# Performance work log

Measured on AMD Instinct MI355X. Metric: run time of the kernel, lower is better.

The kernel has to match this reference:

```python
import jax, jax.numpy as jnp
import numpy as np

N_HEADS = 2
WINDOW = 4
BLOCK = 256


def _get_rel_emb(emb, length):
    # emb: [1, 2*WINDOW+1, K] -> [1, 2*length-1, K]
    pad = max(length - (WINDOW + 1), 0)
    start = max((WINDOW + 1) - length, 0)
    e = jnp.pad(emb, ((0, 0), (pad, pad), (0, 0)))
    return e[:, start:start + 2 * length - 1]


def _rel_to_abs(x):
    # x: [b, h, l, 2l-1] -> [b, h, l, l] (skew trick)
    b, h, l, _ = x.shape
    x = jnp.pad(x, ((0, 0), (0, 0), (0, 0), (0, 1))).reshape(b, h, 2 * l * l)
    x = jnp.pad(x, ((0, 0), (0, 0), (0, l - 1))).reshape(b, h, l + 1, 2 * l - 1)
    return x[:, :, :l, l - 1:]


def _abs_to_rel(x):
    # x: [b, h, l, l] -> [b, h, l, 2l-1] (inverse skew)
    b, h, l, _ = x.shape
    x = jnp.pad(x, ((0, 0), (0, 0), (0, 0), (0, l - 1))).reshape(b, h, l * (2 * l - 1))
    x = jnp.pad(x, ((0, 0), (0, 0), (l, 0))).reshape(b, h, l, 2 * l)
    return x[:, :, :, 1:]


def _attention(x, c, attn_mask, Wq, bq, Wk, bk, Wv, bv, Wo, bo, emb_rel_k, emb_rel_v):
    B, C, T = x.shape
    H, K = N_HEADS, C // N_HEADS
    # projections (torch Linear on [B,T,C])
    q = (jnp.einsum('bct,cd->btd', x, Wq) + bq).reshape(B, T, H, K).transpose(0, 2, 1, 3)
    k = (jnp.einsum('bct,cd->btd', c, Wk) + bk).reshape(B, T, H, K).transpose(0, 2, 1, 3)
    v = (jnp.einsum('bct,cd->btd', c, Wv) + bv).reshape(B, T, H, K).transpose(0, 2, 1, 3)
    qs = q / jnp.sqrt(jnp.float32(K))
    scores = jnp.einsum('bhtk,bhsk->bhts', qs, k)  # [B,H,T,T]
    # relative-position key logits (heads_share=True -> single table)
    rel_k = _get_rel_emb(emb_rel_k, T)[0]          # [2T-1, K]
    rel_logits = jnp.einsum('bhtk,rk->bhtr', qs, rel_k)
    scores = scores + _rel_to_abs(rel_logits)
    # proximal bias: -log1p(|i-j|)
    r = jnp.arange(T, dtype=jnp.float32)
    scores = scores - jnp.log1p(jnp.abs(r[:, None] - r[None, :]))[None, None]
    # attn mask + block-local mask (block mask active because mask is given)
    ij = jnp.arange(T)
    block_ok = jnp.abs(ij[:, None] - ij[None, :]) <= BLOCK
    valid = (attn_mask != 0) & block_ok[None, None]
    scores = jnp.where(valid, scores, jnp.float32(-1e4))
    p = jax.nn.softmax(scores, axis=-1)
    out = jnp.einsum('bhts,bhsk->bhtk', p, v)
    # relative-position value contribution
    rel_v = _get_rel_emb(emb_rel_v, T)[0]          # [2T-1, K]
    out = out + jnp.einsum('bhtr,rk->bhtk', _abs_to_rel(p), rel_v)
    out = out.transpose(0, 2, 1, 3).reshape(B, T, C)
    y = jnp.einsum('btd,do->bto', out, Wo) + bo
    return y.transpose(0, 2, 1)  # [B, out_channels, T]


def setup_inputs() -> dict:
    key = jax.random.key(0)
    ks = jax.random.split(key, 8)
    B, C, T = 4, 192, 2048
    K = C // N_HEADS
    s = jnp.float32(0.05)
    rel_std = jnp.float32(K ** -0.5)
    return {
        'x': jax.random.normal(ks[0], (B, C, T), jnp.float32),
        'c': jax.random.normal(ks[1], (B, C, T), jnp.float32),
        'Wq': jax.random.normal(ks[2], (C, C), jnp.float32) * s,
        'bq': jnp.zeros((C,), jnp.float32),
        'Wk': jax.random.normal(ks[3], (C, C), jnp.float32) * s,
        'bk': jnp.zeros((C,), jnp.float32),
        'Wv': jax.random.normal(ks[4], (C, C), jnp.float32) * s,
        'bv': jnp.zeros((C,), jnp.float32),
        'Wo': jax.random.normal(ks[5], (C, C), jnp.float32) * s,
        'bo': jnp.zeros((C,), jnp.float32),
        'emb_rel_k': jax.random.normal(ks[6], (1, 2 * WINDOW + 1, K), jnp.float32) * rel_std,
        'emb_rel_v': jax.random.normal(ks[7], (1, 2 * WINDOW + 1, K), jnp.float32) * rel_std,
        'attn_mask': jnp.ones((B, 1, T, T), jnp.int32),
    }


def reference(x, c, Wq, bq, Wk, bk, Wv, bv, Wo, bo, emb_rel_k, emb_rel_v, attn_mask):
    return _attention(x, c, attn_mask, Wq, bq, Wk, bk, Wv, bv, Wo, bo, emb_rel_k, emb_rel_v)
```

## Files before the change

### kernel.cpp

```cpp
#include <hip/hip_runtime.h>
#include <hip/hip_bf16.h>

#define B_DIM 4
#define C_DIM 192
#define T_SEQ 2048
#define H_DIM 2
#define K_DIM 96
#define BAND 256
#define IT 16
#define WSLOT 544
#define W_P 548
#define PMW 17

typedef __attribute__((ext_vector_type(8))) short bf16x8;
typedef __attribute__((ext_vector_type(4))) short bf16x4;
typedef __attribute__((ext_vector_type(4))) float f32x4;
#define MFMA16 __builtin_amdgcn_mfma_f32_16x16x32_bf16

__device__ __forceinline__ float bf2f(__hip_bfloat16 v) { return __bfloat162float(v); }
__device__ __forceinline__ float bfbits2f(short s) {
    union { short s; __hip_bfloat16 h; } u; u.s = s; return __bfloat162float(u.h);
}
__device__ __forceinline__ short f2bf_bits(float f) {
    union { __hip_bfloat16 h; short s; } u; u.h = __float2bfloat16(f); return u.s;
}

#define OFF_WT(m)  ((size_t)(m)*73728)
#define OFF_BQS    ((size_t)294912)
#define OFF_PM     ((size_t)295680)
#define OFF_QBF    ((size_t)852736)
#define OFF_KBF    (OFF_QBF + 3145728)
#define OFF_VTB    (OFF_KBF + 3145728)
#define OFF_OBTC   (OFF_VTB + 3145728)

__global__ __launch_bounds__(256)
void prep_w_kernel(const float* __restrict__ Wq, const float* __restrict__ Wk,
                   const float* __restrict__ Wv, const float* __restrict__ Wo,
                   const float* __restrict__ bq, char* __restrict__ ws)
{
    const float qscale = 0.10206207261596577f;
    const size_t idx = (size_t)blockIdx.x*256 + threadIdx.x;
    if (blockIdx.x == 576) {
        if (threadIdx.x < C_DIM)
            ((float*)(ws + OFF_BQS))[threadIdx.x] = bq[threadIdx.x]*qscale;
        return;
    }
    const int mi  = (int)(idx / 36864);
    const int rem = (int)(idx % 36864);
    const int d = rem / C_DIM, c = rem % C_DIM;
    const float* src = (mi == 0) ? Wq : (mi == 1) ? Wk : (mi == 2) ? Wv : Wo;
    float v = src[c*C_DIM + d];
    if (mi == 0) v *= qscale;
    ((short*)(ws + OFF_WT(mi)))[d*C_DIM + c] = f2bf_bits(v);
}

__global__ __launch_bounds__(256)
void pack_mask_kernel(const int* __restrict__ mask, char* __restrict__ ws)
{
    const int idx = blockIdx.x*256 + threadIdx.x;
    const int b = idx / (T_SEQ*PMW);
    const int rem = idx % (T_SEQ*PMW);
    const int i = rem / PMW, w = rem % PMW;
    const int jlo = max(0, (i & ~15) - BAND);
    const int* mrow = mask + ((size_t)b*T_SEQ + i)*T_SEQ;
    unsigned bits = 0;
    #pragma unroll
    for (int g4 = 0; g4 < 8; ++g4) {
        const int jg = jlo + 32*w + 4*g4;
        if (jg + 3 < T_SEQ) {
            const int4 mv = *reinterpret_cast<const int4*>(mrow + jg);
            bits |= (unsigned)(mv.x != 0) << (4*g4);
            bits |= (unsigned)(mv.y != 0) << (4*g4+1);
            bits |= (unsigned)(mv.z != 0) << (4*g4+2);
            bits |= (unsigned)(mv.w != 0) << (4*g4+3);
        } else {
            #pragma unroll
            for (int e = 0; e < 4; ++e)
                if (jg + e < T_SEQ && mrow[jg+e] != 0) bits |= 1u << (4*g4+e);
        }
    }
    ((unsigned*)(ws + OFF_PM))[idx] = bits;
}

__global__ __launch_bounds__(256)
void proj_kernel(const float* __restrict__ x, const float* __restrict__ cin,
                 const float* __restrict__ bk, const float* __restrict__ bv,
                 char* __restrict__ ws)
{
    __shared__ short xs[IT*C_DIM];
    __shared__ short cs[IT*C_DIM];
    const int b   = blockIdx.x >> 7;
    const int t0  = (blockIdx.x & 127) * IT;
    const int tid = threadIdx.x;
    const int wave = tid >> 6, lane = tid & 63;
    const int q4 = lane >> 4, lr = lane & 15;

    if (tid < C_DIM) {
        const int c = tid;
        const float* xp = x   + ((size_t)(b*C_DIM + c))*T_SEQ + t0;
        const float* cp = cin + ((size_t)(b*C_DIM + c))*T_SEQ + t0;
        union { float4 f4[4]; float f[16]; } xu, cu;
        #pragma unroll
        for (int u = 0; u < 4; ++u) {
            xu.f4[u] = *reinterpret_cast<const float4*>(xp + 4*u);
            cu.f4[u] = *reinterpret_cast<const float4*>(cp + 4*u);
        }
        #pragma unroll
        for (int tt = 0; tt < IT; ++tt) {
            xs[tt*C_DIM + c] = f2bf_bits(xu.f[tt]);
            cs[tt*C_DIM + c] = f2bf_bits(cu.f[tt]);
        }
    }
    __syncthreads();

    const short* WqT = (const short*)(ws + OFF_WT(0));
    const short* WkT = (const short*)(ws + OFF_WT(1));
    const short* WvT = (const short*)(ws + OFF_WT(2));

    f32x4 qa[3], ka[3], va[3];
    #pragma unroll
    for (int j = 0; j < 3; ++j) {
        qa[j] = (f32x4){0,0,0,0}; ka[j] = (f32x4){0,0,0,0}; va[j] = (f32x4){0,0,0,0};
    }
    for (int kc = 0; kc < 6; ++kc) {
        const int ko = kc*32 + q4*8;
        const bf16x8 xf = *reinterpret_cast<const bf16x8*>(xs + lr*C_DIM + ko);
        const bf16x8 cf = *reinterpret_cast<const bf16x8*>(cs + lr*C_DIM + ko);
        #pragma unroll
        for (int j = 0; j < 3; ++j) {
            const int dt = 3*wave + j;
            const bf16x8 wqf = *reinterpret_cast<const bf16x8*>(WqT + (dt*16 + lr)*C_DIM + ko);
            const bf16x8 wkf = *reinterpret_cast<const bf16x8*>(WkT + (dt*16 + lr)*C_DIM + ko);
            const bf16x8 wvf = *reinterpret_cast<const bf16x8*>(WvT + (dt*16 + lr)*C_DIM + ko);
            qa[j] = MFMA16(xf, wqf, qa[j], 0, 0, 0);
            ka[j] = MFMA16(cf, wkf, ka[j], 0, 0, 0);
            va[j] = MFMA16(wvf, cf, va[j], 0, 0, 0);
        }
    }

    const float* bqs = (const float*)(ws + OFF_BQS);
    short* qbf = (short*)(ws + OFF_QBF);
    short* kbf = (short*)(ws + OFF_KBF);
    short* vtb = (short*)(ws + OFF_VTB);
    #pragma unroll
    for (int j = 0; j < 3; ++j) {
        const int dt = 3*wave + j;
        {
            const int d = dt*16 + lr, h = d/K_DIM, kk = d%K_DIM;
            const int bh = b*H_DIM + h;
            const float bq_v = bqs[d], bk_v = bk[d];
            #pragma unroll
            for (int e = 0; e < 4; ++e) {
                const int t = t0 + q4*4 + e;
                const size_t off = ((size_t)bh*T_SEQ + t)*K_DIM + kk;
                qbf[off] = f2bf_bits(qa[j][e] + bq_v);
                kbf[off] = f2bf_bits(ka[j][e] + bk_v);
            }
        }
        {
            #pragma unroll
            for (int e = 0; e < 4; ++e) {
                const int d = dt*16 + q4*4 + e, h = d/K_DIM, kk = d%K_DIM;
                const int bh = b*H_DIM + h;
                vtb[((size_t)bh*K_DIM + kk)*T_SEQ + t0 + lr] = f2bf_bits(va[j][e] + bv[d]);
            }
        }
    }
}

__global__ __launch_bounds__(256)
void attn_kernel(const float* __restrict__ relk, const float* __restrict__ relv,
                 char* __restrict__ ws)
{
    __shared__ float p_s[IT*W_P];
    __shared__ float shbuf[864];

    const short* qbf = (const short*)(ws + OFF_QBF);
    const short* kbf = (const short*)(ws + OFF_KBF);
    const short* vtb = (const short*)(ws + OFF_VTB);
    const unsigned* pm = (const unsigned*)(ws + OFF_PM);
    short* obtc = (short*)(ws + OFF_OBTC);

    const int bh  = blockIdx.x >> 7;
    const int i0  = (blockIdx.x & 127) * IT;
    const int b   = bh / H_DIM;
    const int h   = bh % H_DIM;
    const int tid = threadIdx.x;
    const int wave = tid >> 6, lane = tid & 63;
    const int q4 = lane >> 4, lr = lane & 15;

    const int jlo  = max(0, i0 - BAND);
    const int jhi  = min(T_SEQ - 1, i0 + IT - 1 + BAND);
    const int wlen = jhi - jlo + 1;
    const size_t qkv_base = (size_t)bh * T_SEQ * K_DIM;

    float* lt = shbuf;
    float* rl = shbuf + 260;
    for (int idx = tid; idx < 257; idx += 256) lt[idx] = log1pf((float)idx);
    if (tid < IT*9) {
        const int r = tid/9, dd = tid%9;
        const short* qrow = qbf + qkv_base + (size_t)(i0 + r)*K_DIM;
        float s = 0.f;
        for (int k = 0; k < K_DIM; ++k)
            s += bfbits2f(qrow[k]) * relk[dd*K_DIM + k];
        rl[tid] = s;
    }

    bf16x8 qa[3];
    {
        const short* qrow = qbf + qkv_base + (size_t)(i0 + lr)*K_DIM + q4*8;
        #pragma unroll
        for (int kc = 0; kc < 3; ++kc)
            qa[kc] = *reinterpret_cast<const bf16x8*>(qrow + kc*32);
    }

    for (int jt = wave; jt < WSLOT/16; jt += 4) {
        int jr = jlo + jt*16 + lr;
        if (jr > T_SEQ-1) jr = T_SEQ-1;
        const short* krow = kbf + qkv_base + (size_t)jr*K_DIM + q4*8;
        f32x4 s = {0.f,0.f,0.f,0.f};
        #pragma unroll
        for (int kc = 0; kc < 3; ++kc)
            s = MFMA16(qa[kc], *reinterpret_cast<const bf16x8*>(krow + kc*32), s, 0, 0, 0);
        #pragma unroll
        for (int e = 0; e < 4; ++e)
            p_s[(q4*4 + e)*W_P + jt*16 + lr] = s[e];
    }
    __syncthreads();

    {
        const int r = tid >> 4, sj = tid & 15;
        const int i = i0 + r;
        const int pmrow = (b*T_SEQ + i)*PMW;
        float vals[36];
        float m = -INFINITY;
        #pragma unroll
        for (int mm = 0; mm < 9; ++mm) {
            const int j0 = 4*sj + 64*mm;
            float4 pv = make_float4(0.f,0.f,0.f,0.f);
            unsigned mb = 0;
            if (j0 < WSLOT) {
                pv = *reinterpret_cast<const float4*>(p_s + r*W_P + j0);
                mb = pm[pmrow + (j0 >> 5)] >> (j0 & 31);
            }
            const float pe[4] = {pv.x, pv.y, pv.z, pv.w};
            #pragma unroll
            for (int e = 0; e < 4; ++e) {
                const int j = j0 + e;
                float val = -INFINITY;
                if (j0 < WSLOT && j < wlen) {
                    const int jg = jlo + j, dd = jg - i;
                    const int ad = dd < 0 ? -dd : dd;
                    if (ad <= BAND && ((mb >> e) & 1)) {
                        val = pe[e] - lt[ad];
                        if ((unsigned)(dd + 4) <= 8u) val += rl[r*9 + dd + 4];
                    }
                }
                vals[mm*4 + e] = val;
                m = fmaxf(m, val);
            }
        }
        #pragma unroll
        for (int off = 8; off > 0; off >>= 1) m = fmaxf(m, __shfl_xor(m, off, 64));
        if (m == -INFINITY) m = 0.f;
        float ssum = 0.f;
        #pragma unroll
        for (int u = 0; u < 36; ++u) { vals[u] = __expf(vals[u] - m); ssum += vals[u]; }
        #pragma unroll
        for (int off = 8; off > 0; off >>= 1) ssum += __shfl_xor(ssum, off, 64);
        const float inv = ssum > 0.f ? 1.f/ssum : 0.f;
        short* pb = (short*)p_s;
        #pragma unroll
        for (int mm = 0; mm < 9; ++mm) {
            const int j0 = 4*sj + 64*mm;
            if (j0 < WSLOT) {
                bf16x4 w;
                #pragma unroll
                for (int e = 0; e < 4; ++e) w[e] = f2bf_bits(vals[mm*4+e]*inv);
                *reinterpret_cast<bf16x4*>(pb + r*(2*W_P) + j0) = w;
            }
        }
    }
    __syncthreads();

    for (int idx = tid; idx < 9*K_DIM; idx += 256) shbuf[idx] = relv[idx];

    const short* pb = (const short*)p_s;
    f32x4 o0 = {0.f,0.f,0.f,0.f}, o1 = {0.f,0.f,0.f,0.f};
    for (int kc = 0; kc < WSLOT/32; ++kc) {
        const bf16x8 pa = *reinterpret_cast<const bf16x8*>(pb + lr*(2*W_P) + kc*32 + q4*8);
        int tc = jlo + kc*32 + q4*8;
        if (tc > T_SEQ-8) tc = T_SEQ-8;
        const bf16x8 vb0 = *reinterpret_cast<const bf16x8*>(
            vtb + qkv_base + (size_t)(wave*16 + lr)*T_SEQ + tc);
        o0 = MFMA16(pa, vb0, o0, 0, 0, 0);
        if (wave < 2) {
            const bf16x8 vb1 = *reinterpret_cast<const bf16x8*>(
                vtb + qkv_base + (size_t)((wave+4)*16 + lr)*T_SEQ + tc);
            o1 = MFMA16(pa, vb1, o1, 0, 0, 0);
        }
    }
    __syncthreads();

    #pragma unroll
    for (int u = 0; u < 2; ++u) {
        if (u == 1 && wave >= 2) break;
        const int nt = (u == 0) ? wave : wave + 4;
        const f32x4 oc = (u == 0) ? o0 : o1;
        const int col = nt*16 + lr;
        #pragma unroll
        for (int e = 0; e < 4; ++e) {
            const int row = q4*4 + e;
            const int i = i0 + row;
            float v = oc[e];
            #pragma unroll
            for (int dd = 0; dd < 9; ++dd) {
                const int jg = i + dd - 4;
                if (jg >= 0 && jg < T_SEQ)
                    v += bfbits2f(pb[row*(2*W_P) + (jg - jlo)]) * shbuf[dd*K_DIM + col];
            }
            obtc[((size_t)b*T_SEQ + i)*C_DIM + h*K_DIM + col] = f2bf_bits(v);
        }
    }
}

__global__ __launch_bounds__(256)
void oproj_kernel(const float* __restrict__ bo, float* __restrict__ y,
                  const char* __restrict__ ws)
{
    const int b   = blockIdx.x >> 7;
    const int t0  = (blockIdx.x & 127) * 16;
    const int tid = threadIdx.x;
    const int wave = tid >> 6, lane = tid & 63;
    const int q4 = lane >> 4, lr = lane & 15;

    const short* WoT  = (const short*)(ws + OFF_WT(3));
    const short* obtc = (const short*)(ws + OFF_OBTC);

    f32x4 a[3];
    #pragma unroll
    for (int j = 0; j < 3; ++j) a[j] = (f32x4){0.f,0.f,0.f,0.f};
    for (int kc = 0; kc < 6; ++kc) {
        const int ko = kc*32 + q4*8;
        const bf16x8 bf = *reinterpret_cast<const bf16x8*>(
            obtc + ((size_t)b*T_SEQ + t0 + lr)*C_DIM + ko);
        #pragma unroll
        for (int j = 0; j < 3; ++j) {
            const bf16x8 af = *reinterpret_cast<const bf16x8*>(
                WoT + ((3*wave + j)*16 + lr)*C_DIM + ko);
            a[j] = MFMA16(af, bf, a[j], 0, 0, 0);
        }
    }
    #pragma unroll
    for (int j = 0; j < 3; ++j) {
        #pragma unroll
        for (int e = 0; e < 4; ++e) {
            const int d = (3*wave + j)*16 + q4*4 + e;
            y[((size_t)b*C_DIM + d)*T_SEQ + t0 + lr] = a[j][e] + bo[d];
        }
    }
}

extern "C" void kernel_launch(void* const* d_in, const int* in_sizes, int n_in,
                              void* d_out, int out_size, void* d_ws, size_t ws_size,
                              hipStream_t stream)
{
    const float* x    = (const float*)d_in[0];
    const float* c    = (const float*)d_in[1];
    const float* Wq   = (const float*)d_in[2];
    const float* bq   = (const float*)d_in[3];
    const float* Wk   = (const float*)d_in[4];
    const float* bk   = (const float*)d_in[5];
    const float* Wv   = (const float*)d_in[6];
    const float* bv   = (const float*)d_in[7];
    const float* Wo   = (const float*)d_in[8];
    const float* bo   = (const float*)d_in[9];
    const float* relk = (const float*)d_in[10];
    const float* relv = (const float*)d_in[11];
    const int*   mask = (const int*)d_in[12];
    float*       y    = (float*)d_out;
    char*        ws   = (char*)d_ws;

    hipLaunchKernelGGL(prep_w_kernel, dim3(577), dim3(256), 0, stream,
                       Wq, Wk, Wv, Wo, bq, ws);
    hipLaunchKernelGGL(pack_mask_kernel, dim3(544), dim3(256), 0, stream, mask, ws);
    hipLaunchKernelGGL(proj_kernel, dim3(B_DIM*(T_SEQ/16)), dim3(256), 0, stream,
                       x, c, bk, bv, ws);
    hipLaunchKernelGGL(attn_kernel, dim3(B_DIM*H_DIM*(T_SEQ/IT)), dim3(256), 0, stream,
                       relk, relv, ws);
    hipLaunchKernelGGL(oproj_kernel, dim3(B_DIM*(T_SEQ/16)), dim3(256), 0, stream,
                       bo, y, ws);
}
```

Measured before the change: 191.3 us.

## Merge prep kernels, compute relative-key logits with MFMA, spread input loads

Fuses the weight-prep and mask-packing kernels into one launch that also converts the relative-key table to padded bf16. In the attention kernel, the scalar 96-step dot products for the 9 relative-key logits become a single MFMA tile issued by one wave. The projection kernel now spreads its input loads over all 256 threads instead of 192. The weight-transpose index mapping changes so reads are coalesced and writes strided. The intent is to cut launch overhead and serial scalar work, at the cost of one wave doing extra MFMA work and padding the table to 16 rows.

```diff
diff --git a/kernel.cpp b/kernel.cpp
--- a/kernel.cpp
+++ b/kernel.cpp
@@ -17,7 +17,6 @@
 typedef __attribute__((ext_vector_type(4))) float f32x4;
 #define MFMA16 __builtin_amdgcn_mfma_f32_16x16x32_bf16
 
-__device__ __forceinline__ float bf2f(__hip_bfloat16 v) { return __bfloat162float(v); }
 __device__ __forceinline__ float bfbits2f(short s) {
     union { short s; __hip_bfloat16 h; } u; u.s = s; return __bfloat162float(u.h);
 }
@@ -27,59 +26,67 @@
 
 #define OFF_WT(m)  ((size_t)(m)*73728)
 #define OFF_BQS    ((size_t)294912)
-#define OFF_PM     ((size_t)295680)
-#define OFF_QBF    ((size_t)852736)
+#define OFF_RELKBF ((size_t)295680)
+#define OFF_PM     ((size_t)298752)
+#define OFF_QBF    ((size_t)855808)
 #define OFF_KBF    (OFF_QBF + 3145728)
 #define OFF_VTB    (OFF_KBF + 3145728)
 #define OFF_OBTC   (OFF_VTB + 3145728)
 
 __global__ __launch_bounds__(256)
-void prep_w_kernel(const float* __restrict__ Wq, const float* __restrict__ Wk,
-                   const float* __restrict__ Wv, const float* __restrict__ Wo,
-                   const float* __restrict__ bq, char* __restrict__ ws)
+void prep_kernel(const float* __restrict__ Wq, const float* __restrict__ Wk,
+                 const float* __restrict__ Wv, const float* __restrict__ Wo,
+                 const float* __restrict__ bq, const float* __restrict__ relk,
+                 const int* __restrict__ mask, char* __restrict__ ws)
 {
     const float qscale = 0.10206207261596577f;
-    const size_t idx = (size_t)blockIdx.x*256 + threadIdx.x;
-    if (blockIdx.x == 576) {
-        if (threadIdx.x < C_DIM)
-            ((float*)(ws + OFF_BQS))[threadIdx.x] = bq[threadIdx.x]*qscale;
+    const int bidx = blockIdx.x;
+    const int tid  = threadIdx.x;
+
+    if (bidx < 576) {
+        const size_t idx = (size_t)bidx*256 + tid;
+        const int mi  = (int)(idx / 36864);
+        const int rem = (int)(idx % 36864);
+        const int c = rem / C_DIM, d = rem % C_DIM;
+        const float* src = (mi == 0) ? Wq : (mi == 1) ? Wk : (mi == 2) ? Wv : Wo;
+        float v = src[c*C_DIM + d];
+        if (mi == 0) v *= qscale;
+        ((short*)(ws + OFF_WT(mi)))[d*C_DIM + c] = f2bf_bits(v);
         return;
     }
-    const int mi  = (int)(idx / 36864);
-    const int rem = (int)(idx % 36864);
-    const int d = rem / C_DIM, c = rem % C_DIM;
-    const float* src = (mi == 0) ? Wq : (mi == 1) ? Wk : (mi == 2) ? Wv : Wo;
-    float v = src[c*C_DIM + d];
-    if (mi == 0) v *= qscale;
-    ((short*)(ws + OFF_WT(mi)))[d*C_DIM + c] = f2bf_bits(v);
-}
-
-__global__ __launch_bounds__(256)
-void pack_mask_kernel(const int* __restrict__ mask, char* __restrict__ ws)
-{
-    const int idx = blockIdx.x*256 + threadIdx.x;
-    const int b = idx / (T_SEQ*PMW);
-    const int rem = idx % (T_SEQ*PMW);
-    const int i = rem / PMW, w = rem % PMW;
-    const int jlo = max(0, (i & ~15) - BAND);
-    const int* mrow = mask + ((size_t)b*T_SEQ + i)*T_SEQ;
-    unsigned bits = 0;
-    #pragma unroll
-    for (int g4 = 0; g4 < 8; ++g4) {
-        const int jg = jlo + 32*w + 4*g4;
-        if (jg + 3 < T_SEQ) {
-            const int4 mv = *reinterpret_cast<const int4*>(mrow + jg);
-            bits |= (unsigned)(mv.x != 0) << (4*g4);
-            bits |= (unsigned)(mv.y != 0) << (4*g4+1);
-            bits |= (unsigned)(mv.z != 0) << (4*g4+2);
-            bits |= (unsigned)(mv.w != 0) << (4*g4+3);
-        } else {
-            #pragma unroll
-            for (int e = 0; e < 4; ++e)
-                if (jg + e < T_SEQ && mrow[jg+e] != 0) bits |= 1u << (4*g4+e);
-        }
-    }
-    ((unsigned*)(ws + OFF_PM))[idx] = bits;
+    if (bidx < 1120) {
+        const int idx = (bidx - 576)*256 + tid;
+        const int b = idx / (T_SEQ*PMW);
+        const int rem = idx % (T_SEQ*PMW);
+        const int i = rem / PMW, w = rem % PMW;
+        const int jlo = max(0, (i & ~15) - BAND);
+        const int* mrow = mask + ((size_t)b*T_SEQ + i)*T_SEQ;
+        unsigned bits = 0;
+        #pragma unroll
+        for (int g4 = 0; g4 < 8; ++g4) {
+            const int jg = jlo + 32*w + 4*g4;
+            if (jg + 3 < T_SEQ) {
+                const int4 mv = *reinterpret_cast<const int4*>(mrow + jg);
+                bits |= (unsigned)(mv.x != 0) << (4*g4);
+                bits |= (unsigned)(mv.y != 0) << (4*g4+1);
+                bits |= (unsigned)(mv.z != 0) << (4*g4+2);
+                bits |= (unsigned)(mv.w != 0) << (4*g4+3);
+            } else {
+                #pragma unroll
+                for (int e = 0; e < 4; ++e)
+                    if (jg + e < T_SEQ && mrow[jg+e] != 0) bits |= 1u << (4*g4+e);
+            }
+        }
+        ((unsigned*)(ws + OFF_PM))[idx] = bits;
+        return;
+    }
+    if (tid < C_DIM)
+        ((float*)(ws + OFF_BQS))[tid] = bq[tid]*qscale;
+    short* rkb = (short*)(ws + OFF_RELKBF);
+    for (int idx = tid; idx < 16*K_DIM; idx += 256) {
+        const int row = idx / K_DIM;
+        rkb[idx] = (row < 9) ? f2bf_bits(relk[idx]) : (short)0;
+    }
 }
 
 __global__ __launch_bounds__(256)
@@ -95,21 +102,19 @@
     const int wave = tid >> 6, lane = tid & 63;
     const int q4 = lane >> 4, lr = lane & 15;
 
-    if (tid < C_DIM) {
-        const int c = tid;
-        const float* xp = x   + ((size_t)(b*C_DIM + c))*T_SEQ + t0;
-        const float* cp = cin + ((size_t)(b*C_DIM + c))*T_SEQ + t0;
-        union { float4 f4[4]; float f[16]; } xu, cu;
-        #pragma unroll
-        for (int u = 0; u < 4; ++u) {
-            xu.f4[u] = *reinterpret_cast<const float4*>(xp + 4*u);
-            cu.f4[u] = *reinterpret_cast<const float4*>(cp + 4*u);
-        }
-        #pragma unroll
-        for (int tt = 0; tt < IT; ++tt) {
-            xs[tt*C_DIM + c] = f2bf_bits(xu.f[tt]);
-            cs[tt*C_DIM + c] = f2bf_bits(cu.f[tt]);
-        }
+    for (int l = tid; l < 768; l += 256) {
+        const int cr = l >> 2, u = l & 3;
+        const size_t off = (size_t)(b*C_DIM + cr)*T_SEQ + t0 + 4*u;
+        const float4 xv = *reinterpret_cast<const float4*>(x + off);
+        const float4 cv = *reinterpret_cast<const float4*>(cin + off);
+        xs[(4*u+0)*C_DIM + cr] = f2bf_bits(xv.x);
+        xs[(4*u+1)*C_DIM + cr] = f2bf_bits(xv.y);
+        xs[(4*u+2)*C_DIM + cr] = f2bf_bits(xv.z);
+        xs[(4*u+3)*C_DIM + cr] = f2bf_bits(xv.w);
+        cs[(4*u+0)*C_DIM + cr] = f2bf_bits(cv.x);
+        cs[(4*u+1)*C_DIM + cr] = f2bf_bits(cv.y);
+        cs[(4*u+2)*C_DIM + cr] = f2bf_bits(cv.z);
+        cs[(4*u+3)*C_DIM + cr] = f2bf_bits(cv.w);
     }
     __syncthreads();
 
@@ -169,8 +174,7 @@
 }
 
 __global__ __launch_bounds__(256)
-void attn_kernel(const float* __restrict__ relk, const float* __restrict__ relv,
-                 char* __restrict__ ws)
+void attn_kernel(const float* __restrict__ relv, char* __restrict__ ws)
 {
     __shared__ float p_s[IT*W_P];
     __shared__ float shbuf[864];
@@ -178,6 +182,7 @@
     const short* qbf = (const short*)(ws + OFF_QBF);
     const short* kbf = (const short*)(ws + OFF_KBF);
     const short* vtb = (const short*)(ws + OFF_VTB);
+    const short* rkb = (const short*)(ws + OFF_RELKBF);
     const unsigned* pm = (const unsigned*)(ws + OFF_PM);
     short* obtc = (short*)(ws + OFF_OBTC);
 
@@ -197,14 +202,6 @@
     float* lt = shbuf;
     float* rl = shbuf + 260;
     for (int idx = tid; idx < 257; idx += 256) lt[idx] = log1pf((float)idx);
-    if (tid < IT*9) {
-        const int r = tid/9, dd = tid%9;
-        const short* qrow = qbf + qkv_base + (size_t)(i0 + r)*K_DIM;
-        float s = 0.f;
-        for (int k = 0; k < K_DIM; ++k)
-            s += bfbits2f(qrow[k]) * relk[dd*K_DIM + k];
-        rl[tid] = s;
-    }
 
     bf16x8 qa[3];
     {
@@ -225,6 +222,18 @@
         #pragma unroll
         for (int e = 0; e < 4; ++e)
             p_s[(q4*4 + e)*W_P + jt*16 + lr] = s[e];
+    }
+    if (wave == 3) {
+        const short* krow = rkb + lr*K_DIM + q4*8;
+        f32x4 s = {0.f,0.f,0.f,0.f};
+        #pragma unroll
+        for (int kc = 0; kc < 3; ++kc)
+            s = MFMA16(qa[kc], *reinterpret_cast<const bf16x8*>(krow + kc*32), s, 0, 0, 0);
+        if (lr < 9) {
+            #pragma unroll
+            for (int e = 0; e < 4; ++e)
+                rl[(q4*4 + e)*9 + lr] = s[e];
+        }
     }
     __syncthreads();
 
@@ -381,13 +390,12 @@
     float*       y    = (float*)d_out;
     char*        ws   = (char*)d_ws;
 
-    hipLaunchKernelGGL(prep_w_kernel, dim3(577), dim3(256), 0, stream,
-                       Wq, Wk, Wv, Wo, bq, ws);
-    hipLaunchKernelGGL(pack_mask_kernel, dim3(544), dim3(256), 0, stream, mask, ws);
+    hipLaunchKernelGGL(prep_kernel, dim3(1121), dim3(256), 0, stream,
+                       Wq, Wk, Wv, Wo, bq, relk, mask, ws);
     hipLaunchKernelGGL(proj_kernel, dim3(B_DIM*(T_SEQ/16)), dim3(256), 0, stream,
                        x, c, bk, bv, ws);
     hipLaunchKernelGGL(attn_kernel, dim3(B_DIM*H_DIM*(T_SEQ/IT)), dim3(256), 0, stream,
-                       relk, relv, ws);
+                       relv, ws);
     hipLaunchKernelGGL(oproj_kernel, dim3(B_DIM*(T_SEQ/16)), dim3(256), 0, stream,
                        bo, y, ws);
 }
```

New measurement: 179.8 us. 6.0% less time.
